# Optimization experiments

Hardware: AMD Instinct MI355X
Metric: run time of the kernel (lower is better)

Reference implementation:

```python
import jax, jax.numpy as jnp
import numpy as np

B, T, K = 256, 512, 128          # batch, seq_len, n_tag
START, STOP = 126, 127           # tag2idx[START_TAG], tag2idx[STOP_TAG]
NEG = -10000.0                   # same constant the torch module uses


def setup_inputs() -> dict:
    key = jax.random.key(0)
    k1, k2, k3 = jax.random.split(key, 3)
    feats = jax.random.normal(k1, (B, T, K), dtype=jnp.float32)
    tags = jax.random.randint(k2, (B, T), 0, 126)  # never START/STOP
    # learned CRF transition matrix: trans[to, from]
    transitions = 0.1 * jax.random.normal(k3, (K, K), dtype=jnp.float32)
    transitions = transitions.at[START, :].set(NEG).at[:, STOP].set(NEG)
    return {"feats": feats, "tags": tags, "transitions": transitions}


def _forward_alg(feats, trans):
    """Batched CRF forward algorithm. feats [B,T,K] -> log Z [B]."""
    b = feats.shape[0]
    init = jnp.full((b, K), NEG, feats.dtype).at[:, START].set(0.0)

    def step(alpha, feat_t):
        # scores[b, to, from] = alpha[b, from] + trans[to, from]
        scores = alpha[:, None, :] + trans[None, :, :]
        alpha_new = jax.nn.logsumexp(scores, axis=-1) + feat_t
        return alpha_new, None

    alpha, _ = jax.lax.scan(step, init, jnp.swapaxes(feats, 0, 1))
    return jax.nn.logsumexp(alpha + trans[STOP][None, :], axis=-1)


def _score_sentence(feats, tags, trans):
    """Batched gold path score. feats [B,T,K], tags [B,T] -> [B]."""
    b = feats.shape[0]
    start_col = jnp.full((b, 1), START, tags.dtype)
    tags_ext = jnp.concatenate([start_col, tags], axis=1)      # [B,T+1]
    trans_sc = trans[tags_ext[:, 1:], tags_ext[:, :-1]].sum(axis=1)
    emit_sc = jnp.take_along_axis(feats, tags[..., None], axis=2)[..., 0].sum(axis=1)
    return trans_sc + emit_sc + trans[STOP, tags[:, -1]]


def _viterbi(feats, trans):
    """Batched Viterbi decode. Returns (path_score [B], path [B,T])."""
    b = feats.shape[0]
    init = jnp.full((b, K), NEG, feats.dtype).at[:, START].set(0.0)

    def step(alpha, feat_t):
        scores = alpha[:, None, :] + trans[None, :, :]   # [B,to,from]
        bptr = jnp.argmax(scores, axis=-1)               # [B,to]
        alpha_new = jnp.max(scores, axis=-1) + feat_t
        return alpha_new, bptr

    alpha, bptrs = jax.lax.scan(step, init, jnp.swapaxes(feats, 0, 1))
    term = alpha + trans[STOP][None, :]
    last_tag = jnp.argmax(term, axis=-1)                 # [B]
    path_score = jnp.max(term, axis=-1)

    def back(tag_t, bp_t):
        prev = jnp.take_along_axis(bp_t, tag_t[:, None], axis=1)[:, 0]
        return prev, tag_t

    _, path = jax.lax.scan(back, last_tag, bptrs, reverse=True)  # [T,B]
    return path_score, jnp.swapaxes(path, 0, 1)


def reference(feats, tags, transitions):
    log_z = _forward_alg(feats, transitions)             # forward_alg per sentence
    gold = _score_sentence(feats, tags, transitions)     # score_sentence
    path_score, pred = _viterbi(feats, transitions)      # viterbi_decode
    loss = jnp.sum(log_z - gold) / jnp.float32(feats.shape[0] * feats.shape[1])
    return loss, path_score, pred
```

## Files before the change

### kernel.cpp

```cpp
#include <hip/hip_runtime.h>
#include <cstdint>
#include <cstddef>

#define BB 256
#define TT 512
#define KK 128
#define START_TAG 126
#define STOP_TAG 127
#define NEGV (-10000.0f)
#define NINF (-__builtin_huge_valf())

template<int CTRL>
__device__ __forceinline__ float dppf(float v, float old) {
  return __int_as_float(__builtin_amdgcn_update_dpp(
      __float_as_int(old), __float_as_int(v), CTRL, 0xf, 0xf, false));
}
template<int CTRL>
__device__ __forceinline__ int dppi(int v, int old) {
  return __builtin_amdgcn_update_dpp(old, v, CTRL, 0xf, 0xf, false);
}
__device__ __forceinline__ float wave_max63(float x) {
  x = fmaxf(x, dppf<0x111>(x, NINF));
  x = fmaxf(x, dppf<0x112>(x, NINF));
  x = fmaxf(x, dppf<0x114>(x, NINF));
  x = fmaxf(x, dppf<0x118>(x, NINF));
  x = fmaxf(x, dppf<0x142>(x, NINF));
  x = fmaxf(x, dppf<0x143>(x, NINF));
  return x;
}
__device__ __forceinline__ int paddr(int i) { return (i >> 5) * 36 + (i & 31); }

template<bool CHEAP>
__global__ __launch_bounds__(768) void crf_main(
    const float* __restrict__ feats, const float* __restrict__ trans,
    float* __restrict__ logz, float* __restrict__ pscore,
    int* __restrict__ lasttag, uint8_t* __restrict__ bptr,
    float* __restrict__ alphaS)
{
  const int b = blockIdx.x;
  const int tid = threadIdx.x;
  const bool is_fwd = tid < 256;
  const int lane = tid & 63;

  __shared__ __align__(16) float P[2][144];
  __shared__ __align__(16) float AV[2][144];
  __shared__ __align__(16) float redmF[2][4];
  __shared__ float reds[4];
  __shared__ float vitm[8];
  __shared__ int   viti[8];

  int myto, h;
  if (is_fwd) { myto = tid >> 1; h = tid & 1; }
  else { int q = tid - 256; myto = q >> 2; h = q & 3; }

  float R[64];
  if (is_fwd) {
    const float4* tr = (const float4*)(trans + (size_t)myto * KK + h * 64);
#pragma unroll
    for (int c = 0; c < 16; ++c) {
      float4 v = tr[c];
      R[4*c+0]=__expf(v.x); R[4*c+1]=__expf(v.y);
      R[4*c+2]=__expf(v.z); R[4*c+3]=__expf(v.w);
    }
  } else {
    const float4* tr = (const float4*)(trans + (size_t)myto * KK + h * 32);
#pragma unroll
    for (int c = 0; c < 8; ++c) {
      float4 v = tr[c];
      R[4*c+0]=v.x; R[4*c+1]=v.y; R[4*c+2]=v.z; R[4*c+3]=v.w;
    }
  }

  if (is_fwd) { if (h == 0) P[0][paddr(myto)] = (myto==START_TAG)?1.0f:0.0f; }
  else        { if (h == 0) AV[0][paddr(myto)] = (myto==START_TAG)?0.0f:NEGV; }
  if (tid < 4) redmF[1][tid] = 0.0f;
  __syncthreads();

  const float* fb = feats + (size_t)b * TT * KK + myto;
  uint8_t* bp = bptr + (size_t)b * TT * KK + myto;
  float* aS = alphaS + (size_t)b * TT * KK;

  float fcur = fb[0];
  float Mprev = 0.0f;
  float aCarry = 0.0f;
  int cur = 0;

  for (int t = 0; t < TT; ++t) {
    const int tn = (t + 1 < TT) ? t + 1 : t;
    float fnext = fb[(size_t)tn * KK];
    const int rd = (t + 1) & 1, wr = t & 1;

    if (is_fwd) {
      float4 rv = *(const float4*)&redmF[rd][0];
      float M1 = fmaxf(fmaxf(rv.x, rv.y), fmaxf(rv.z, rv.w));
      const float* Pc = &P[cur][0];
      const int base = h * 72;
      float s0=0.f, s1=0.f, s2=0.f, s3=0.f;
#pragma unroll
      for (int c = 0; c < 16; ++c) {
        float4 p = *(const float4*)&Pc[base + (c>>3)*36 + (c&7)*4];
        s0 = fmaf(R[4*c+0], p.x, s0);
        s1 = fmaf(R[4*c+1], p.y, s1);
        s2 = fmaf(R[4*c+2], p.z, s2);
        s3 = fmaf(R[4*c+3], p.w, s3);
      }
      float s = (s0 + s1) + (s2 + s3);
      s = s + dppf<0xB1>(s, s);
      float a;
      if (CHEAP) a = Mprev + __logf(s) + fcur;
      else       a = Mprev + logf(s) + fcur;
      float wm = wave_max63(a);
      if (lane == 63) redmF[wr][tid >> 6] = wm;
      float pv = CHEAP ? __expf(a - M1) : expf(a - M1);
      if (h == 0) P[cur ^ 1][paddr(myto)] = pv;
      Mprev = M1;
      aCarry = a;
    } else if (CHEAP) {
      const float* Ac = &AV[cur][0];
      const int base = h * 36;
      float4 p0 = *(const float4*)&Ac[base];
      float m0 = p0.x + R[0], m1 = p0.y + R[1];
      float m2 = p0.z + R[2], m3 = p0.w + R[3];
#pragma unroll
      for (int c = 1; c < 8; ++c) {
        float4 p = *(const float4*)&Ac[base + c*4];
        m0 = fmaxf(m0, p.x + R[4*c+0]);
        m1 = fmaxf(m1, p.y + R[4*c+1]);
        m2 = fmaxf(m2, p.z + R[4*c+2]);
        m3 = fmaxf(m3, p.w + R[4*c+3]);
      }
      float m = fmaxf(fmaxf(m0, m1), fmaxf(m2, m3));
      m = fmaxf(m, dppf<0xB1>(m, m));
      m = fmaxf(m, dppf<0x4E>(m, m));
      float a = m + fcur;
      if (h == 0) {
        AV[cur ^ 1][paddr(myto)] = a;
        __builtin_nontemporal_store(a, &aS[(size_t)t * KK + myto]);
      }
      aCarry = a;
    } else {
      const float* Ac = &AV[cur][0];
      const int base = h * 36;
      const int fb0 = h * 32;
      float4 p0 = *(const float4*)&Ac[base];
      float m0 = p0.x + R[0], m1 = p0.y + R[1], m2 = p0.z + R[2], m3 = p0.w + R[3];
      int i0 = fb0, i1 = fb0+1, i2 = fb0+2, i3 = fb0+3;
#pragma unroll
      for (int c = 1; c < 8; ++c) {
        float4 p = *(const float4*)&Ac[base + c*4];
        float v0 = p.x + R[4*c+0]; if (v0 > m0) { m0 = v0; i0 = fb0+4*c+0; }
        float v1 = p.y + R[4*c+1]; if (v1 > m1) { m1 = v1; i1 = fb0+4*c+1; }
        float v2 = p.z + R[4*c+2]; if (v2 > m2) { m2 = v2; i2 = fb0+4*c+2; }
        float v3 = p.w + R[4*c+3]; if (v3 > m3) { m3 = v3; i3 = fb0+4*c+3; }
      }
      float m = m0; int i = i0;
      if (m1 > m || (m1 == m && i1 < i)) { m = m1; i = i1; }
      if (m2 > m || (m2 == m && i2 < i)) { m = m2; i = i2; }
      if (m3 > m || (m3 == m && i3 < i)) { m = m3; i = i3; }
      { float mo = dppf<0xB1>(m, m); int io = dppi<0xB1>(i, i);
        if (mo > m || (mo == m && io < i)) { m = mo; i = io; } }
      { float mo = dppf<0x4E>(m, m); int io = dppi<0x4E>(i, i);
        if (mo > m || (mo == m && io < i)) { m = mo; i = io; } }
      float a = m + fcur;
      if (h == 0) { AV[cur ^ 1][paddr(myto)] = a; bp[(size_t)t * KK] = (uint8_t)i; }
      aCarry = a;
    }
    __syncthreads();
    cur ^= 1;
    fcur = fnext;
  }

  float tstop = trans[(size_t)STOP_TAG * KK + myto];
  float term = aCarry + tstop;
  float M = 0.0f;
  if (is_fwd) {
    float wm = wave_max63(term);
    if (lane == 63) redmF[0][tid >> 6] = wm;
  } else {
    float m = term; int i = myto;
#pragma unroll
    for (int off = 1; off < 64; off <<= 1) {
      float mo = __shfl_xor(m, off, 64);
      int   io = __shfl_xor(i, off, 64);
      if (mo > m || (mo == m && io < i)) { m = mo; i = io; }
    }
    if (lane == 0) { vitm[(tid>>6)-4] = m; viti[(tid>>6)-4] = i; }
  }
  __syncthreads();
  if (is_fwd) {
    float4 rv = *(const float4*)&redmF[0][0];
    M = fmaxf(fmaxf(rv.x, rv.y), fmaxf(rv.z, rv.w));
    float e = CHEAP ? __expf(term - M) : expf(term - M);
#pragma unroll
    for (int off = 1; off < 64; off <<= 1) e += __shfl_xor(e, off, 64);
    if (lane == 0) reds[tid >> 6] = e;
  } else if (tid == 256) {
    float m = vitm[0]; int i = viti[0];
#pragma unroll
    for (int w = 1; w < 8; ++w)
      if (vitm[w] > m || (vitm[w] == m && viti[w] < i)) { m = vitm[w]; i = viti[w]; }
    pscore[b] = m; lasttag[b] = i;
  }
  __syncthreads();
  if (tid == 0) {
    float sm = reds[0] + reds[1] + reds[2] + reds[3];
    logz[b] = M + (CHEAP ? __logf(sm) : logf(sm));
  }
}

__global__ __launch_bounds__(64) void backtrace_alpha(
    const float* __restrict__ alphaS, const float* __restrict__ trans,
    const int* __restrict__ lasttag, float* __restrict__ pred)
{
  const int b = blockIdx.x;
  const int lane = threadIdx.x;
  __shared__ float tl[KK * KK];
  {
    const float4* src = (const float4*)trans;
    float4* dst = (float4*)tl;
#pragma unroll
    for (int i = 0; i < (KK * KK / 4) / 64; ++i) dst[lane + i * 64] = src[lane + i * 64];
  }
  int tag = lasttag[b];
  if (lane == 0) pred[(size_t)b * TT + (TT - 1)] = (float)tag;
  const float* arow = alphaS + (size_t)b * TT * KK;

  float p0[8], p1[8];
#pragma unroll
  for (int j = 0; j < 8; ++j) {
    int r = TT - 2 - j;
    p0[j] = arow[(size_t)r * KK + lane];
    p1[j] = arow[(size_t)r * KK + 64 + lane];
  }
  __syncthreads();

  for (int rb = TT - 2; rb >= 0; rb -= 8) {
#pragma unroll
    for (int j = 0; j < 8; ++j) {
      int r = rb - j;
      if (r >= 0) {
        float x0 = p0[j] + tl[tag * KK + lane];
        float x1 = p1[j] + tl[tag * KK + 64 + lane];
        float m = fmaxf(x0, x1);
        float M = wave_max63(m);
        M = __int_as_float(__builtin_amdgcn_readlane(__float_as_int(M), 63));
        unsigned long long b0 = __ballot(x0 == M);
        unsigned long long b1 = __ballot(x1 == M);
        tag = b0 ? (int)__builtin_ctzll(b0) : 64 + (int)__builtin_ctzll(b1);
        if (lane == 0) pred[(size_t)b * TT + r] = (float)tag;
        int rp = r - 8;
        if (rp >= 0) {
          p0[j] = arow[(size_t)rp * KK + lane];
          p1[j] = arow[(size_t)rp * KK + 64 + lane];
        }
      }
    }
  }
}

__global__ __launch_bounds__(256) void backtrace_kernel(
    const uint8_t* __restrict__ bptr, const int* __restrict__ lasttag,
    float* __restrict__ pred)
{
  const int b = blockIdx.x;
  const int tid = threadIdx.x;
  __shared__ __align__(16) uint8_t lb[(TT / 2) * KK];
  __shared__ int tagcarry;
  if (tid == 0) tagcarry = lasttag[b];

  for (int half = 1; half >= 0; --half) {
    __syncthreads();
    const float4* src = reinterpret_cast<const float4*>(
        bptr + ((size_t)b * TT + (size_t)half * (TT / 2)) * KK);
    float4* dst = reinterpret_cast<float4*>(lb);
    for (int i = tid; i < (TT / 2) * KK / 16; i += 256) dst[i] = src[i];
    __syncthreads();
    if (tid == 0) {
      int tag = tagcarry;
      for (int t = TT / 2 - 1; t >= 0; --t) {
        int gt = half * (TT / 2) + t;
        pred[(size_t)b * TT + gt] = (float)tag;
        tag = lb[t * KK + tag];
      }
      tagcarry = tag;
    }
  }
}

__global__ __launch_bounds__(64) void gold_kernel(
    const float* __restrict__ feats, const int* __restrict__ tags,
    const float* __restrict__ trans, const float* __restrict__ logz,
    float* __restrict__ gb)
{
  const int b = blockIdx.x;
  const int lane = threadIdx.x;
  const int* tg = tags + (size_t)b * TT;
  const float* fb = feats + (size_t)b * TT * KK;
  float g = 0.0f;
#pragma unroll
  for (int k = 0; k < TT / 64; ++k) {
    int t = lane * (TT / 64) + k;
    int ct = tg[t];
    int pv = (t == 0) ? START_TAG : tg[t - 1];
    g += trans[ct * KK + pv] + fb[(size_t)t * KK + ct];
  }
  if (lane == 63) g += trans[STOP_TAG * KK + tg[TT - 1]];
#pragma unroll
  for (int off = 1; off <= 32; off <<= 1) g += __shfl_xor(g, off, 64);
  if (lane == 0) gb[b] = logz[b] - g;
}

__global__ __launch_bounds__(256) void loss_reduce(
    const float* __restrict__ gb, float* __restrict__ out)
{
  const int tid = threadIdx.x;
  const int lane = tid & 63, wv = tid >> 6;
  float v = gb[tid];
#pragma unroll
  for (int off = 1; off <= 32; off <<= 1) v += __shfl_xor(v, off, 64);
  __shared__ float red[4];
  if (lane == 0) red[wv] = v;
  __syncthreads();
  if (tid == 0) out[0] = (red[0] + red[1] + red[2] + red[3]) / (float)(BB * TT);
}

extern "C" void kernel_launch(void* const* d_in, const int* in_sizes, int n_in,
                              void* d_out, int out_size, void* d_ws, size_t ws_size,
                              hipStream_t stream) {
  const float* feats = (const float*)d_in[0];
  const int*   tags  = (const int*)d_in[1];
  const float* trans = (const float*)d_in[2];

  float* out    = (float*)d_out;
  float* loss   = out;
  float* pscore = out + 1;
  float* pred   = out + 1 + BB;
  (void)in_sizes; (void)n_in; (void)out_size;

  const size_t alpha_bytes = (size_t)BB * TT * KK * sizeof(float);
  const bool cheap = ws_size >= alpha_bytes + 4096;

  if (cheap) {
    float* alphaS  = (float*)d_ws;
    char*  wsend   = (char*)d_ws + alpha_bytes;
    float* logz    = (float*)(wsend);
    int*   lasttag = (int*)(wsend + BB * sizeof(float));
    float* gb      = (float*)(wsend + BB * sizeof(float) + BB * sizeof(int));
    crf_main<true><<<BB, 768, 0, stream>>>(feats, trans, logz, pscore, lasttag,
                                           (uint8_t*)nullptr, alphaS);
    backtrace_alpha<<<BB, 64, 0, stream>>>(alphaS, trans, lasttag, pred);
    gold_kernel<<<BB, 64, 0, stream>>>(feats, tags, trans, logz, gb);
    loss_reduce<<<1, 256, 0, stream>>>(gb, loss);
  } else {
    uint8_t* bptr    = (uint8_t*)d_ws;
    char*    wsend   = (char*)d_ws + (size_t)BB * TT * KK;
    float*   logz    = (float*)(wsend);
    int*     lasttag = (int*)(wsend + BB * sizeof(float));
    float*   gb      = (float*)(wsend + BB * sizeof(float) + BB * sizeof(int));
    crf_main<false><<<BB, 768, 0, stream>>>(feats, trans, logz, pscore, lasttag,
                                            bptr, (float*)nullptr);
    backtrace_kernel<<<BB, 256, 0, stream>>>(bptr, lasttag, pred);
    gold_kernel<<<BB, 64, 0, stream>>>(feats, tags, trans, logz, gb);
    loss_reduce<<<1, 256, 0, stream>>>(gb, loss);
  }
}
```

Before: 426.0 us.

## Split forward and Viterbi into separate blocks and fuse gold score

The combined 768-thread block, which ran forward-algorithm and Viterbi waves side by side, becomes a 2*B-block launch. The first B blocks run Viterbi and the rest run the forward algorithm, each with 512 threads using 4 lanes per tag. The gold-path score is folded into the forward blocks, so the separate gold_kernel launch and the logz round trip go away. The goal is to double block-level parallelism across CUs and drop one launch, at the cost of each block doing a full sequential recurrence on its own. The non-cheap fallback keeps the old kernel.

```diff
diff --git a/kernel.cpp b/kernel.cpp
--- a/kernel.cpp
+++ b/kernel.cpp
@@ -30,75 +30,128 @@
 }
 __device__ __forceinline__ int paddr(int i) { return (i >> 5) * 36 + (i & 31); }
 
-template<bool CHEAP>
-__global__ __launch_bounds__(768) void crf_main(
+__global__ __launch_bounds__(512) void crf_uber(
     const float* __restrict__ feats, const float* __restrict__ trans,
-    float* __restrict__ logz, float* __restrict__ pscore,
-    int* __restrict__ lasttag, uint8_t* __restrict__ bptr,
-    float* __restrict__ alphaS)
+    const int* __restrict__ tags,
+    float* __restrict__ pscore, int* __restrict__ lasttag,
+    float* __restrict__ alphaS, float* __restrict__ gb)
 {
-  const int b = blockIdx.x;
+  const int bid = blockIdx.x;
   const int tid = threadIdx.x;
-  const bool is_fwd = tid < 256;
   const int lane = tid & 63;
-
-  __shared__ __align__(16) float P[2][144];
-  __shared__ __align__(16) float AV[2][144];
-  __shared__ __align__(16) float redmF[2][4];
-  __shared__ float reds[4];
+  const int wv = tid >> 6;
+  const int myto = tid >> 2;
+  const int h = tid & 3;
+
+  __shared__ __align__(16) float BUF[2][144];
+  __shared__ __align__(16) float redmF[2][8];
+  __shared__ float reds[8];
+  __shared__ float redg[8];
   __shared__ float vitm[8];
   __shared__ int   viti[8];
 
-  int myto, h;
-  if (is_fwd) { myto = tid >> 1; h = tid & 1; }
-  else { int q = tid - 256; myto = q >> 2; h = q & 3; }
-
-  float R[64];
-  if (is_fwd) {
-    const float4* tr = (const float4*)(trans + (size_t)myto * KK + h * 64);
-#pragma unroll
-    for (int c = 0; c < 16; ++c) {
-      float4 v = tr[c];
-      R[4*c+0]=__expf(v.x); R[4*c+1]=__expf(v.y);
-      R[4*c+2]=__expf(v.z); R[4*c+3]=__expf(v.w);
+  if (bid < BB) {
+    const int b = bid;
+    float R[32];
+    {
+      const float4* tr = (const float4*)(trans + (size_t)myto * KK + h * 32);
+#pragma unroll
+      for (int c = 0; c < 8; ++c) {
+        float4 v = tr[c];
+        R[4*c+0]=v.x; R[4*c+1]=v.y; R[4*c+2]=v.z; R[4*c+3]=v.w;
+      }
+    }
+    if (h == 0) BUF[0][paddr(myto)] = (myto == START_TAG) ? 0.0f : NEGV;
+    __syncthreads();
+
+    const float* fb = feats + (size_t)b * TT * KK + myto;
+    float* aS = alphaS + (size_t)b * TT * KK;
+    float fcur = fb[0];
+    float a = 0.0f;
+    int cur = 0;
+
+    for (int t = 0; t < TT; ++t) {
+      const int tn = (t + 1 < TT) ? t + 1 : t;
+      float fnext = fb[(size_t)tn * KK];
+      const float* Ac = &BUF[cur][0];
+      const int base = h * 36;
+      float4 p0 = *(const float4*)&Ac[base];
+      float m0 = fmaxf(p0.x + R[0], p0.y + R[1]);
+      float m1 = fmaxf(p0.z + R[2], p0.w + R[3]);
+#pragma unroll
+      for (int c = 1; c < 8; ++c) {
+        float4 p = *(const float4*)&Ac[base + c * 4];
+        m0 = fmaxf(fmaxf(m0, p.x + R[4*c+0]), p.y + R[4*c+1]);
+        m1 = fmaxf(fmaxf(m1, p.z + R[4*c+2]), p.w + R[4*c+3]);
+      }
+      float m = fmaxf(m0, m1);
+      m = fmaxf(m, dppf<0xB1>(m, m));
+      m = fmaxf(m, dppf<0x4E>(m, m));
+      a = m + fcur;
+      if (h == 0) {
+        BUF[cur ^ 1][paddr(myto)] = a;
+        __builtin_nontemporal_store(a, &aS[(size_t)t * KK + myto]);
+      }
+      __syncthreads();
+      cur ^= 1;
+      fcur = fnext;
+    }
+
+    float term = a + trans[(size_t)STOP_TAG * KK + myto];
+    float m = term; int i = myto;
+#pragma unroll
+    for (int off = 1; off < 64; off <<= 1) {
+      float mo = __shfl_xor(m, off, 64);
+      int   io = __shfl_xor(i, off, 64);
+      if (mo > m || (mo == m && io < i)) { m = mo; i = io; }
+    }
+    if (lane == 0) { vitm[wv] = m; viti[wv] = i; }
+    __syncthreads();
+    if (tid == 0) {
+      float mm = vitm[0]; int ii = viti[0];
+#pragma unroll
+      for (int w = 1; w < 8; ++w)
+        if (vitm[w] > mm || (vitm[w] == mm && viti[w] < ii)) { mm = vitm[w]; ii = viti[w]; }
+      pscore[b] = mm; lasttag[b] = ii;
     }
   } else {
-    const float4* tr = (const float4*)(trans + (size_t)myto * KK + h * 32);
-#pragma unroll
-    for (int c = 0; c < 8; ++c) {
-      float4 v = tr[c];
-      R[4*c+0]=v.x; R[4*c+1]=v.y; R[4*c+2]=v.z; R[4*c+3]=v.w;
-    }
-  }
-
-  if (is_fwd) { if (h == 0) P[0][paddr(myto)] = (myto==START_TAG)?1.0f:0.0f; }
-  else        { if (h == 0) AV[0][paddr(myto)] = (myto==START_TAG)?0.0f:NEGV; }
-  if (tid < 4) redmF[1][tid] = 0.0f;
-  __syncthreads();
-
-  const float* fb = feats + (size_t)b * TT * KK + myto;
-  uint8_t* bp = bptr + (size_t)b * TT * KK + myto;
-  float* aS = alphaS + (size_t)b * TT * KK;
-
-  float fcur = fb[0];
-  float Mprev = 0.0f;
-  float aCarry = 0.0f;
-  int cur = 0;
-
-  for (int t = 0; t < TT; ++t) {
-    const int tn = (t + 1 < TT) ? t + 1 : t;
-    float fnext = fb[(size_t)tn * KK];
-    const int rd = (t + 1) & 1, wr = t & 1;
-
-    if (is_fwd) {
-      float4 rv = *(const float4*)&redmF[rd][0];
-      float M1 = fmaxf(fmaxf(rv.x, rv.y), fmaxf(rv.z, rv.w));
-      const float* Pc = &P[cur][0];
-      const int base = h * 72;
-      float s0=0.f, s1=0.f, s2=0.f, s3=0.f;
-#pragma unroll
-      for (int c = 0; c < 16; ++c) {
-        float4 p = *(const float4*)&Pc[base + (c>>3)*36 + (c&7)*4];
+    const int b = bid - BB;
+    float R[32];
+    {
+      const float4* tr = (const float4*)(trans + (size_t)myto * KK + h * 32);
+#pragma unroll
+      for (int c = 0; c < 8; ++c) {
+        float4 v = tr[c];
+        R[4*c+0]=__expf(v.x); R[4*c+1]=__expf(v.y);
+        R[4*c+2]=__expf(v.z); R[4*c+3]=__expf(v.w);
+      }
+    }
+    if (h == 0) BUF[0][paddr(myto)] = (myto == START_TAG) ? 1.0f : 0.0f;
+    if (tid < 8) redmF[1][tid] = 0.0f;
+    __syncthreads();
+
+    const float* fb = feats + (size_t)b * TT * KK + myto;
+    float fcur = fb[0];
+    float Mprev = 0.0f;
+    float a = 0.0f;
+    int cur = 0;
+
+    for (int t = 0; t < TT; ++t) {
+      const int tn = (t + 1 < TT) ? t + 1 : t;
+      float fnext = fb[(size_t)tn * KK];
+      const int rd = (t + 1) & 1, wr = t & 1;
+
+      float4 r0 = *(const float4*)&redmF[rd][0];
+      float4 r1 = *(const float4*)&redmF[rd][4];
+      float M1 = fmaxf(fmaxf(fmaxf(r0.x, r0.y), fmaxf(r0.z, r0.w)),
+                       fmaxf(fmaxf(r1.x, r1.y), fmaxf(r1.z, r1.w)));
+
+      const float* Pc = &BUF[cur][0];
+      const int base = h * 36;
+      float s0 = 0.f, s1 = 0.f, s2 = 0.f, s3 = 0.f;
+#pragma unroll
+      for (int c = 0; c < 8; ++c) {
+        float4 p = *(const float4*)&Pc[base + c * 4];
         s0 = fmaf(R[4*c+0], p.x, s0);
         s1 = fmaf(R[4*c+1], p.y, s1);
         s2 = fmaf(R[4*c+2], p.z, s2);
@@ -106,105 +159,47 @@
       }
       float s = (s0 + s1) + (s2 + s3);
       s = s + dppf<0xB1>(s, s);
-      float a;
-      if (CHEAP) a = Mprev + __logf(s) + fcur;
-      else       a = Mprev + logf(s) + fcur;
+      s = s + dppf<0x4E>(s, s);
+      a = Mprev + __logf(s) + fcur;
       float wm = wave_max63(a);
-      if (lane == 63) redmF[wr][tid >> 6] = wm;
-      float pv = CHEAP ? __expf(a - M1) : expf(a - M1);
-      if (h == 0) P[cur ^ 1][paddr(myto)] = pv;
+      if (lane == 63) redmF[wr][wv] = wm;
+      float pv = __expf(a - M1);
+      if (h == 0) BUF[cur ^ 1][paddr(myto)] = pv;
       Mprev = M1;
-      aCarry = a;
-    } else if (CHEAP) {
-      const float* Ac = &AV[cur][0];
-      const int base = h * 36;
-      float4 p0 = *(const float4*)&Ac[base];
-      float m0 = p0.x + R[0], m1 = p0.y + R[1];
-      float m2 = p0.z + R[2], m3 = p0.w + R[3];
-#pragma unroll
-      for (int c = 1; c < 8; ++c) {
-        float4 p = *(const float4*)&Ac[base + c*4];
-        m0 = fmaxf(m0, p.x + R[4*c+0]);
-        m1 = fmaxf(m1, p.y + R[4*c+1]);
-        m2 = fmaxf(m2, p.z + R[4*c+2]);
-        m3 = fmaxf(m3, p.w + R[4*c+3]);
-      }
-      float m = fmaxf(fmaxf(m0, m1), fmaxf(m2, m3));
-      m = fmaxf(m, dppf<0xB1>(m, m));
-      m = fmaxf(m, dppf<0x4E>(m, m));
-      float a = m + fcur;
-      if (h == 0) {
-        AV[cur ^ 1][paddr(myto)] = a;
-        __builtin_nontemporal_store(a, &aS[(size_t)t * KK + myto]);
-      }
-      aCarry = a;
-    } else {
-      const float* Ac = &AV[cur][0];
-      const int base = h * 36;
-      const int fb0 = h * 32;
-      float4 p0 = *(const float4*)&Ac[base];
-      float m0 = p0.x + R[0], m1 = p0.y + R[1], m2 = p0.z + R[2], m3 = p0.w + R[3];
-      int i0 = fb0, i1 = fb0+1, i2 = fb0+2, i3 = fb0+3;
-#pragma unroll
-      for (int c = 1; c < 8; ++c) {
-        float4 p = *(const float4*)&Ac[base + c*4];
-        float v0 = p.x + R[4*c+0]; if (v0 > m0) { m0 = v0; i0 = fb0+4*c+0; }
-        float v1 = p.y + R[4*c+1]; if (v1 > m1) { m1 = v1; i1 = fb0+4*c+1; }
-        float v2 = p.z + R[4*c+2]; if (v2 > m2) { m2 = v2; i2 = fb0+4*c+2; }
-        float v3 = p.w + R[4*c+3]; if (v3 > m3) { m3 = v3; i3 = fb0+4*c+3; }
-      }
-      float m = m0; int i = i0;
-      if (m1 > m || (m1 == m && i1 < i)) { m = m1; i = i1; }
-      if (m2 > m || (m2 == m && i2 < i)) { m = m2; i = i2; }
-      if (m3 > m || (m3 == m && i3 < i)) { m = m3; i = i3; }
-      { float mo = dppf<0xB1>(m, m); int io = dppi<0xB1>(i, i);
-        if (mo > m || (mo == m && io < i)) { m = mo; i = io; } }
-      { float mo = dppf<0x4E>(m, m); int io = dppi<0x4E>(i, i);
-        if (mo > m || (mo == m && io < i)) { m = mo; i = io; } }
-      float a = m + fcur;
-      if (h == 0) { AV[cur ^ 1][paddr(myto)] = a; bp[(size_t)t * KK] = (uint8_t)i; }
-      aCarry = a;
-    }
-    __syncthreads();
-    cur ^= 1;
-    fcur = fnext;
-  }
-
-  float tstop = trans[(size_t)STOP_TAG * KK + myto];
-  float term = aCarry + tstop;
-  float M = 0.0f;
-  if (is_fwd) {
+      __syncthreads();
+      cur ^= 1;
+      fcur = fnext;
+    }
+
+    float term = a + trans[(size_t)STOP_TAG * KK + myto];
     float wm = wave_max63(term);
-    if (lane == 63) redmF[0][tid >> 6] = wm;
-  } else {
-    float m = term; int i = myto;
-#pragma unroll
-    for (int off = 1; off < 64; off <<= 1) {
-      float mo = __shfl_xor(m, off, 64);
-      int   io = __shfl_xor(i, off, 64);
-      if (mo > m || (mo == m && io < i)) { m = mo; i = io; }
-    }
-    if (lane == 0) { vitm[(tid>>6)-4] = m; viti[(tid>>6)-4] = i; }
-  }
-  __syncthreads();
-  if (is_fwd) {
-    float4 rv = *(const float4*)&redmF[0][0];
-    M = fmaxf(fmaxf(rv.x, rv.y), fmaxf(rv.z, rv.w));
-    float e = CHEAP ? __expf(term - M) : expf(term - M);
+    if (lane == 63) redmF[0][wv] = wm;
+    __syncthreads();
+    float4 r0 = *(const float4*)&redmF[0][0];
+    float4 r1 = *(const float4*)&redmF[0][4];
+    float M = fmaxf(fmaxf(fmaxf(r0.x, r0.y), fmaxf(r0.z, r0.w)),
+                    fmaxf(fmaxf(r1.x, r1.y), fmaxf(r1.z, r1.w)));
+    float e = (h == 0) ? __expf(term - M) : 0.0f;
 #pragma unroll
     for (int off = 1; off < 64; off <<= 1) e += __shfl_xor(e, off, 64);
-    if (lane == 0) reds[tid >> 6] = e;
-  } else if (tid == 256) {
-    float m = vitm[0]; int i = viti[0];
-#pragma unroll
-    for (int w = 1; w < 8; ++w)
-      if (vitm[w] > m || (vitm[w] == m && viti[w] < i)) { m = vitm[w]; i = viti[w]; }
-    pscore[b] = m; lasttag[b] = i;
-  }
-  __syncthreads();
-  if (tid == 0) {
-    float sm = reds[0] + reds[1] + reds[2] + reds[3];
-    logz[b] = M + (CHEAP ? __logf(sm) : logf(sm));
+    if (lane == 0) reds[wv] = e;
+
+    const int* tg = tags + (size_t)b * TT;
+    const float* fg = feats + (size_t)b * TT * KK;
+    int ct = tg[tid];
+    int pv2 = (tid == 0) ? START_TAG : tg[tid - 1];
+    float g = trans[(size_t)ct * KK + pv2] + fg[(size_t)tid * KK + ct];
+    if (tid == TT - 1) g += trans[(size_t)STOP_TAG * KK + ct];
+#pragma unroll
+    for (int off = 1; off < 64; off <<= 1) g += __shfl_xor(g, off, 64);
+    if (lane == 0) redg[wv] = g;
+    __syncthreads();
+    if (tid == 0) {
+      float se = reds[0]+reds[1]+reds[2]+reds[3]+reds[4]+reds[5]+reds[6]+reds[7];
+      float sg = redg[0]+redg[1]+redg[2]+redg[3]+redg[4]+redg[5]+redg[6]+redg[7];
+      float logzv = M + __logf(se);
+      gb[b] = logzv - sg;
+    }
   }
 }
 
@@ -258,6 +253,166 @@
   }
 }
 
+__global__ __launch_bounds__(256) void loss_reduce(
+    const float* __restrict__ gb, float* __restrict__ out)
+{
+  const int tid = threadIdx.x;
+  const int lane = tid & 63, wv = tid >> 6;
+  float v = gb[tid];
+#pragma unroll
+  for (int off = 1; off <= 32; off <<= 1) v += __shfl_xor(v, off, 64);
+  __shared__ float red[4];
+  if (lane == 0) red[wv] = v;
+  __syncthreads();
+  if (tid == 0) out[0] = (red[0] + red[1] + red[2] + red[3]) / (float)(BB * TT);
+}
+
+__global__ __launch_bounds__(768) void crf_main_fb(
+    const float* __restrict__ feats, const float* __restrict__ trans,
+    float* __restrict__ logz, float* __restrict__ pscore,
+    int* __restrict__ lasttag, uint8_t* __restrict__ bptr)
+{
+  const int b = blockIdx.x;
+  const int tid = threadIdx.x;
+  const bool is_fwd = tid < 256;
+  const int lane = tid & 63;
+
+  __shared__ __align__(16) float P[2][144];
+  __shared__ __align__(16) float AV[2][144];
+  __shared__ __align__(16) float redmF[2][4];
+  __shared__ float reds[4];
+  __shared__ float vitm[8];
+  __shared__ int   viti[8];
+
+  int myto, h;
+  if (is_fwd) { myto = tid >> 1; h = tid & 1; }
+  else { int q = tid - 256; myto = q >> 2; h = q & 3; }
+
+  float R[64];
+  if (is_fwd) {
+    const float4* tr = (const float4*)(trans + (size_t)myto * KK + h * 64);
+#pragma unroll
+    for (int c = 0; c < 16; ++c) {
+      float4 v = tr[c];
+      R[4*c+0]=expf(v.x); R[4*c+1]=expf(v.y); R[4*c+2]=expf(v.z); R[4*c+3]=expf(v.w);
+    }
+  } else {
+    const float4* tr = (const float4*)(trans + (size_t)myto * KK + h * 32);
+#pragma unroll
+    for (int c = 0; c < 8; ++c) {
+      float4 v = tr[c];
+      R[4*c+0]=v.x; R[4*c+1]=v.y; R[4*c+2]=v.z; R[4*c+3]=v.w;
+    }
+  }
+
+  if (is_fwd) { if (h == 0) P[0][paddr(myto)] = (myto==START_TAG)?1.0f:0.0f; }
+  else        { if (h == 0) AV[0][paddr(myto)] = (myto==START_TAG)?0.0f:NEGV; }
+  if (tid < 4) redmF[1][tid] = 0.0f;
+  __syncthreads();
+
+  const float* fb = feats + (size_t)b * TT * KK + myto;
+  uint8_t* bp = bptr + (size_t)b * TT * KK + myto;
+
+  float fcur = fb[0];
+  float Mprev = 0.0f;
+  float aCarry = 0.0f;
+  int cur = 0;
+
+  for (int t = 0; t < TT; ++t) {
+    const int tn = (t + 1 < TT) ? t + 1 : t;
+    float fnext = fb[(size_t)tn * KK];
+    const int rd = (t + 1) & 1, wr = t & 1;
+
+    if (is_fwd) {
+      float4 rv = *(const float4*)&redmF[rd][0];
+      float M1 = fmaxf(fmaxf(rv.x, rv.y), fmaxf(rv.z, rv.w));
+      const float* Pc = &P[cur][0];
+      const int base = h * 72;
+      float s0=0.f, s1=0.f, s2=0.f, s3=0.f;
+#pragma unroll
+      for (int c = 0; c < 16; ++c) {
+        float4 p = *(const float4*)&Pc[base + (c>>3)*36 + (c&7)*4];
+        s0 = fmaf(R[4*c+0], p.x, s0);
+        s1 = fmaf(R[4*c+1], p.y, s1);
+        s2 = fmaf(R[4*c+2], p.z, s2);
+        s3 = fmaf(R[4*c+3], p.w, s3);
+      }
+      float s = (s0 + s1) + (s2 + s3);
+      s = s + dppf<0xB1>(s, s);
+      float a = Mprev + logf(s) + fcur;
+      float wm = wave_max63(a);
+      if (lane == 63) redmF[wr][tid >> 6] = wm;
+      float pv = expf(a - M1);
+      if (h == 0) P[cur ^ 1][paddr(myto)] = pv;
+      Mprev = M1;
+      aCarry = a;
+    } else {
+      const float* Ac = &AV[cur][0];
+      const int base = h * 36;
+      const int fb0 = h * 32;
+      float4 p0 = *(const float4*)&Ac[base];
+      float m0 = p0.x + R[0], m1 = p0.y + R[1], m2 = p0.z + R[2], m3 = p0.w + R[3];
+      int i0 = fb0, i1 = fb0+1, i2 = fb0+2, i3 = fb0+3;
+#pragma unroll
+      for (int c = 1; c < 8; ++c) {
+        float4 p = *(const float4*)&Ac[base + c*4];
+        float v0 = p.x + R[4*c+0]; if (v0 > m0) { m0 = v0; i0 = fb0+4*c+0; }
+        float v1 = p.y + R[4*c+1]; if (v1 > m1) { m1 = v1; i1 = fb0+4*c+1; }
+        float v2 = p.z + R[4*c+2]; if (v2 > m2) { m2 = v2; i2 = fb0+4*c+2; }
+        float v3 = p.w + R[4*c+3]; if (v3 > m3) { m3 = v3; i3 = fb0+4*c+3; }
+      }
+      float m = m0; int i = i0;
+      if (m1 > m || (m1 == m && i1 < i)) { m = m1; i = i1; }
+      if (m2 > m || (m2 == m && i2 < i)) { m = m2; i = i2; }
+      if (m3 > m || (m3 == m && i3 < i)) { m = m3; i = i3; }
+      { float mo = dppf<0xB1>(m, m); int io = dppi<0xB1>(i, i);
+        if (mo > m || (mo == m && io < i)) { m = mo; i = io; } }
+      { float mo = dppf<0x4E>(m, m); int io = dppi<0x4E>(i, i);
+        if (mo > m || (mo == m && io < i)) { m = mo; i = io; } }
+      float a = m + fcur;
+      if (h == 0) { AV[cur ^ 1][paddr(myto)] = a; bp[(size_t)t * KK] = (uint8_t)i; }
+      aCarry = a;
+    }
+    __syncthreads();
+    cur ^= 1;
+    fcur = fnext;
+  }
+
+  float tstop = trans[(size_t)STOP_TAG * KK + myto];
+  float term = aCarry + tstop;
+  float M = 0.0f;
+  if (is_fwd) {
+    float wm = wave_max63(term);
+    if (lane == 63) redmF[0][tid >> 6] = wm;
+  } else {
+    float m = term; int i = myto;
+#pragma unroll
+    for (int off = 1; off < 64; off <<= 1) {
+      float mo = __shfl_xor(m, off, 64);
+      int   io = __shfl_xor(i, off, 64);
+      if (mo > m || (mo == m && io < i)) { m = mo; i = io; }
+    }
+    if (lane == 0) { vitm[(tid>>6)-4] = m; viti[(tid>>6)-4] = i; }
+  }
+  __syncthreads();
+  if (is_fwd) {
+    float4 rv = *(const float4*)&redmF[0][0];
+    M = fmaxf(fmaxf(rv.x, rv.y), fmaxf(rv.z, rv.w));
+    float e = (h == 0) ? expf(term - M) : 0.0f;
+#pragma unroll
+    for (int off = 1; off < 64; off <<= 1) e += __shfl_xor(e, off, 64);
+    if (lane == 0) reds[tid >> 6] = e;
+  } else if (tid == 256) {
+    float m = vitm[0]; int i = viti[0];
+#pragma unroll
+    for (int w = 1; w < 8; ++w)
+      if (vitm[w] > m || (vitm[w] == m && viti[w] < i)) { m = vitm[w]; i = viti[w]; }
+    pscore[b] = m; lasttag[b] = i;
+  }
+  __syncthreads();
+  if (tid == 0) logz[b] = M + logf(reds[0] + reds[1] + reds[2] + reds[3]);
+}
+
 __global__ __launch_bounds__(256) void backtrace_kernel(
     const uint8_t* __restrict__ bptr, const int* __restrict__ lasttag,
     float* __restrict__ pred)
@@ -310,20 +465,6 @@
   if (lane == 0) gb[b] = logz[b] - g;
 }
 
-__global__ __launch_bounds__(256) void loss_reduce(
-    const float* __restrict__ gb, float* __restrict__ out)
-{
-  const int tid = threadIdx.x;
-  const int lane = tid & 63, wv = tid >> 6;
-  float v = gb[tid];
-#pragma unroll
-  for (int off = 1; off <= 32; off <<= 1) v += __shfl_xor(v, off, 64);
-  __shared__ float red[4];
-  if (lane == 0) red[wv] = v;
-  __syncthreads();
-  if (tid == 0) out[0] = (red[0] + red[1] + red[2] + red[3]) / (float)(BB * TT);
-}
-
 extern "C" void kernel_launch(void* const* d_in, const int* in_sizes, int n_in,
                               void* d_out, int out_size, void* d_ws, size_t ws_size,
                               hipStream_t stream) {
@@ -343,13 +484,11 @@
   if (cheap) {
     float* alphaS  = (float*)d_ws;
     char*  wsend   = (char*)d_ws + alpha_bytes;
-    float* logz    = (float*)(wsend);
-    int*   lasttag = (int*)(wsend + BB * sizeof(float));
-    float* gb      = (float*)(wsend + BB * sizeof(float) + BB * sizeof(int));
-    crf_main<true><<<BB, 768, 0, stream>>>(feats, trans, logz, pscore, lasttag,
-                                           (uint8_t*)nullptr, alphaS);
+    int*   lasttag = (int*)(wsend);
+    float* gb      = (float*)(wsend + BB * sizeof(int));
+    crf_uber<<<2 * BB, 512, 0, stream>>>(feats, trans, tags, pscore, lasttag,
+                                         alphaS, gb);
     backtrace_alpha<<<BB, 64, 0, stream>>>(alphaS, trans, lasttag, pred);
-    gold_kernel<<<BB, 64, 0, stream>>>(feats, tags, trans, logz, gb);
     loss_reduce<<<1, 256, 0, stream>>>(gb, loss);
   } else {
     uint8_t* bptr    = (uint8_t*)d_ws;
@@ -357,8 +496,7 @@
     float*   logz    = (float*)(wsend);
     int*     lasttag = (int*)(wsend + BB * sizeof(float));
     float*   gb      = (float*)(wsend + BB * sizeof(float) + BB * sizeof(int));
-    crf_main<false><<<BB, 768, 0, stream>>>(feats, trans, logz, pscore, lasttag,
-                                            bptr, (float*)nullptr);
+    crf_main_fb<<<BB, 768, 0, stream>>>(feats, trans, logz, pscore, lasttag, bptr);
     backtrace_kernel<<<BB, 256, 0, stream>>>(bptr, lasttag, pred);
     gold_kernel<<<BB, 64, 0, stream>>>(feats, tags, trans, logz, gb);
     loss_reduce<<<1, 256, 0, stream>>>(gb, loss);
```

New measurement: 440.4 us. 3.4% more time.
